# Kernel optimization log

Measured on AMD Instinct MI355X. Metric: run time of the kernel, lower is better.

The kernel has to match this reference:

```python
import jax, jax.numpy as jnp
import numpy as np

N = 50000      # nodes
E = 800000     # edges (before self-loops)
D = 128        # hid_d
H = 8          # heads
C = D // H     # per-head channels
L = 3          # layers
SLOPE = 0.2    # GATv2 leaky_relu negative slope
EPS = 1e-5     # LayerNorm eps


def setup_inputs() -> dict:
    key = jax.random.key(0)
    ks = jax.random.split(key, 8)
    x = jax.random.normal(ks[0], (N, D), dtype=jnp.float32)
    ei = jax.random.randint(ks[1], (2, E), 0, N, dtype=jnp.int32)
    s = 1.0 / np.sqrt(D)
    Wl = jax.random.normal(ks[2], (L, D, D), dtype=jnp.float32) * s   # source transform per layer
    Wr = jax.random.normal(ks[3], (L, D, D), dtype=jnp.float32) * s   # target transform per layer
    att = jax.random.normal(ks[4], (L, H, C), dtype=jnp.float32) * (1.0 / np.sqrt(C))
    bias = jnp.zeros((L, D), dtype=jnp.float32)
    gamma = jnp.ones((L, D), dtype=jnp.float32)
    beta = jnp.zeros((L, D), dtype=jnp.float32)
    return {"x": x, "Wl": Wl, "Wr": Wr, "att": att, "bias": bias,
            "gamma": gamma, "beta": beta, "ei": ei}


def _layernorm(y, g, b):
    mu = jnp.mean(y, axis=-1, keepdims=True)
    var = jnp.mean(jnp.square(y - mu), axis=-1, keepdims=True)
    return (y - mu) * jax.lax.rsqrt(var + EPS) * g + b


def reference(x, Wl, Wr, att, bias, gamma, beta, ei):
    # append self-loops (PyG GATv2Conv default add_self_loops=True)
    loops = jnp.arange(N, dtype=ei.dtype)
    src = jnp.concatenate([ei[0], loops])  # [E+N]
    dst = jnp.concatenate([ei[1], loops])  # [E+N]
    h = x
    for l in range(L):
        xl = (h @ Wl[l]).reshape(N, H, C)   # source-side features
        xr = (h @ Wr[l]).reshape(N, H, C)   # target-side features
        feat = xl[src] + xr[dst]            # [E+N, H, C] per-edge gather
        logits = jnp.einsum('ehc,hc->eh', jax.nn.leaky_relu(feat, SLOPE), att[l])
        # segment softmax over incoming edges of each dst node
        m = jax.ops.segment_max(logits, dst, num_segments=N)
        ex = jnp.exp(logits - m[dst])
        denom = jax.ops.segment_sum(ex, dst, num_segments=N)
        alpha = ex / denom[dst]             # [E+N, H]
        msg = alpha[:, :, None] * xl[src]   # [E+N, H, C]
        out = jax.ops.segment_sum(msg, dst, num_segments=N).reshape(N, H * C) + bias[l]
        # wrapper: h = h + dropout(elu(norm(gat(h)))) ; dropout = identity (eval)
        h = h + jax.nn.elu(_layernorm(out, gamma[l], beta[l]))
    return h
```

## Files before the change

### kernel.cpp

```cpp
#include <hip/hip_runtime.h>
#include <hip/hip_fp16.h>
#include <math.h>

#define N_NODES 50000
#define N_EDGES 800000
#define D 128
#define L 3
#define SLOPE 0.2f
#define LN_EPS 1e-5f
#define ETOT (N_EDGES + N_NODES)
#define SCAN_BLOCKS ((N_NODES + 1023) / 1024)

typedef _Float16 half8 __attribute__((ext_vector_type(8)));
typedef _Float16 h2v  __attribute__((ext_vector_type(2)));
typedef float f32x4 __attribute__((ext_vector_type(4)));


__global__ void rank_hist_kernel(const int* __restrict__ ei, int* __restrict__ counts,
                                 int* __restrict__ rank) {
    int idx = blockIdx.x * blockDim.x + threadIdx.x;
    if (idx >= ETOT) return;
    int d = (idx < N_EDGES) ? ei[N_EDGES + idx] : (idx - N_EDGES);
    rank[idx] = atomicAdd(&counts[d], 1);
}

__global__ __launch_bounds__(1024) void scan1_kernel(const int* __restrict__ counts,
                                                     int* __restrict__ offsets,
                                                     int* __restrict__ bsum) {
    __shared__ int wsum[16];
    int tid = threadIdx.x;
    int lane = tid & 63, w = tid >> 6;
    int i = blockIdx.x * 1024 + tid;
    int v = (i < N_NODES) ? counts[i] : 0;
    int sc = v;
    #pragma unroll
    for (int off = 1; off < 64; off <<= 1) {
        int u = __shfl_up(sc, off);
        if (lane >= off) sc += u;
    }
    if (lane == 63) wsum[w] = sc;
    __syncthreads();
    if (w == 0) {
        int t2 = (lane < 16) ? wsum[lane] : 0;
        #pragma unroll
        for (int off = 1; off < 16; off <<= 1) {
            int u = __shfl_up(t2, off);
            if (lane >= off) t2 += u;
        }
        if (lane < 16) wsum[lane] = t2;
    }
    __syncthreads();
    int wpref = (w == 0) ? 0 : wsum[w - 1];
    if (i < N_NODES) offsets[i] = wpref + sc - v;
    if (tid == 0) bsum[blockIdx.x] = wsum[15];
}

__global__ __launch_bounds__(64) void scan2_kernel(const int* __restrict__ bsum,
                                                   int* __restrict__ bpre) {
    int lane = threadIdx.x;
    int v = (lane < SCAN_BLOCKS) ? bsum[lane] : 0;
    int sc = v;
    #pragma unroll
    for (int off = 1; off < 64; off <<= 1) {
        int u = __shfl_up(sc, off);
        if (lane >= off) sc += u;
    }
    if (lane < SCAN_BLOCKS) bpre[lane] = sc - v;
}

__global__ __launch_bounds__(1024) void scan3_kernel(int* __restrict__ offsets,
                                                     const int* __restrict__ bpre) {
    int i = blockIdx.x * 1024 + threadIdx.x;
    if (i < N_NODES) offsets[i] += bpre[blockIdx.x];
    if (i == 0) offsets[N_NODES] = ETOT;
}

__global__ void scatter_kernel(const int* __restrict__ ei, const int* __restrict__ offsets,
                               const int* __restrict__ rank,
                               unsigned short* __restrict__ sorted16) {
    int idx = blockIdx.x * blockDim.x + threadIdx.x;
    if (idx >= ETOT) return;
    int s, d;
    if (idx < N_EDGES) { s = ei[idx]; d = ei[N_EDGES + idx]; }
    else               { s = d = idx - N_EDGES; }
    sorted16[offsets[d] + rank[idx]] = (unsigned short)s;
}


__global__ __launch_bounds__(256) void wfrag_kernel(const float* __restrict__ Wl,
                                                    const float* __restrict__ Wr,
                                                    _Float16* __restrict__ Wfrag) {
    int u = blockIdx.x * 256 + threadIdx.x;
    if (u >= 3 * 4096) return;
    int lane = u & 63, nt = (u >> 6) & 7, kt = (u >> 9) & 3, y = (u >> 11) & 1, l = u >> 12;
    int r = lane & 15, q = lane >> 4;
    const float* W = (y ? Wr : Wl) + (size_t)l * D * D;
    half8 v;
    #pragma unroll
    for (int j = 0; j < 8; ++j)
        v[j] = (_Float16)W[(kt * 32 + q * 8 + j) * D + nt * 16 + r];
    *(half8*)&Wfrag[(size_t)u * 8] = v;
}


__global__ __launch_bounds__(256) void gemm_mfma_kernel(
        const float* __restrict__ h, const _Float16* __restrict__ WfragL,
        _Float16* __restrict__ xlh, _Float16* __restrict__ xrh) {
    __shared__ half8 Afrag[1024];
    int t = threadIdx.x;
    int row0 = blockIdx.x * 64;
    {
        int kt = t >> 6, q = (t >> 4) & 3, r = t & 15;
        int kc = kt * 4 + q;
        #pragma unroll
        for (int i = 0; i < 4; ++i) {
            int row = row0 + i * 16 + r;
            float4 f0 = make_float4(0.f, 0.f, 0.f, 0.f), f1 = f0;
            if (row < N_NODES) {
                const float* p = &h[(size_t)row * D + kc * 8];
                f0 = *(const float4*)p;
                f1 = *(const float4*)(p + 4);
            }
            half8 v;
            v[0] = (_Float16)f0.x; v[1] = (_Float16)f0.y;
            v[2] = (_Float16)f0.z; v[3] = (_Float16)f0.w;
            v[4] = (_Float16)f1.x; v[5] = (_Float16)f1.y;
            v[6] = (_Float16)f1.z; v[7] = (_Float16)f1.w;
            Afrag[i * 256 + t] = v;
        }
    }
    __syncthreads();
    int w = t >> 6, lane = t & 63;
    f32x4 acc[16];
    #pragma unroll
    for (int i = 0; i < 16; ++i) acc[i] = (f32x4){0.f, 0.f, 0.f, 0.f};
    #pragma unroll
    for (int kt = 0; kt < 4; ++kt) {
        half8 a = Afrag[(w * 4 + kt) * 64 + lane];
        #pragma unroll
        for (int y = 0; y < 2; ++y) {
            #pragma unroll
            for (int nt = 0; nt < 8; ++nt) {
                half8 b = *(const half8*)&WfragL[(size_t)(((y * 4 + kt) * 8 + nt) * 64 + lane) * 8];
                acc[y * 8 + nt] = __builtin_amdgcn_mfma_f32_16x16x32_f16(a, b, acc[y * 8 + nt], 0, 0, 0);
            }
        }
    }
    int rq = lane >> 4, rc = lane & 15;
    int rbase = row0 + w * 16 + rq * 4;
    #pragma unroll
    for (int y = 0; y < 2; ++y) {
        _Float16* out = y ? xrh : xlh;
        #pragma unroll
        for (int nt = 0; nt < 8; ++nt) {
            #pragma unroll
            for (int reg = 0; reg < 4; ++reg) {
                int row = rbase + reg;
                if (row < N_NODES)
                    out[(size_t)row * D + nt * 16 + rc] = (_Float16)acc[y * 8 + nt][reg];
            }
        }
    }
}


__device__ __forceinline__ float head_reduce8(float p) {
    int t;
    t = __builtin_amdgcn_update_dpp(0, __float_as_int(p), 0xB1, 0xF, 0xF, true);
    p += __int_as_float(t);
    t = __builtin_amdgcn_update_dpp(0, __float_as_int(p), 0x4E, 0xF, 0xF, true);
    p += __int_as_float(t);
    t = __builtin_amdgcn_update_dpp(0, __float_as_int(p), 0x141, 0xF, 0xF, true);
    p += __int_as_float(t);
    return p;
}

__device__ __forceinline__ float logit2(h2v v, h2v xrv2, h2v att2, h2v slope2) {
    h2v f  = v + xrv2;
    h2v lf = __builtin_elementwise_max(f, f * slope2);
    return __builtin_amdgcn_fdot2(lf, att2, 0.f, false);
}

__device__ __forceinline__ float2 h2f(h2v v) {
    return make_float2((float)v[0], (float)v[1]);
}

__global__ __launch_bounds__(256) void gat_node_kernel(
        const _Float16* __restrict__ xlh, const _Float16* __restrict__ xrh,
        const int* __restrict__ offsets, const unsigned short* __restrict__ sorted16,
        const float* __restrict__ att_l, const float* __restrict__ bias_l,
        const float* __restrict__ gamma_l, const float* __restrict__ beta_l,
        const float* __restrict__ hin, float* __restrict__ hout) {
    int node = (blockIdx.x * blockDim.x + threadIdx.x) >> 6;
    if (node >= N_NODES) return;
    int lane = threadIdx.x & 63;
    unsigned laneoff = lane * 4u;
    h2v xrv2 = ((const h2v*)xrh)[(size_t)node * 64 + lane];
    float2 attf = *(const float2*)&att_l[2 * lane];
    h2v att2;
    att2[0] = (_Float16)(attf.x * 1.44269504f);
    att2[1] = (_Float16)(attf.y * 1.44269504f);
    h2v slope2;
    slope2[0] = (_Float16)SLOPE;
    slope2[1] = (_Float16)SLOPE;
    int beg = offsets[node], end = offsets[node + 1];
    float s = 0.f, accx = 0.f, accy = 0.f;
    const char* xlb = (const char*)xlh;
    for (int c0 = beg; c0 < end; c0 += 64) {
        int cnt = end - c0; if (cnt > 64) cnt = 64;
        unsigned idx = sorted16[c0 + (lane < cnt ? lane : cnt - 1)];
        unsigned off = idx << 8;
        int j = 0;
        for (; j + 8 <= cnt; j += 8) {
            unsigned o0 = __builtin_amdgcn_readlane(off, j)     + laneoff;
            unsigned o1 = __builtin_amdgcn_readlane(off, j + 1) + laneoff;
            unsigned o2 = __builtin_amdgcn_readlane(off, j + 2) + laneoff;
            unsigned o3 = __builtin_amdgcn_readlane(off, j + 3) + laneoff;
            unsigned o4 = __builtin_amdgcn_readlane(off, j + 4) + laneoff;
            unsigned o5 = __builtin_amdgcn_readlane(off, j + 5) + laneoff;
            unsigned o6 = __builtin_amdgcn_readlane(off, j + 6) + laneoff;
            unsigned o7 = __builtin_amdgcn_readlane(off, j + 7) + laneoff;
            h2v v0 = *(const h2v*)(xlb + o0);
            h2v v1 = *(const h2v*)(xlb + o1);
            h2v v2 = *(const h2v*)(xlb + o2);
            h2v v3 = *(const h2v*)(xlb + o3);
            h2v v4 = *(const h2v*)(xlb + o4);
            h2v v5 = *(const h2v*)(xlb + o5);
            h2v v6 = *(const h2v*)(xlb + o6);
            h2v v7 = *(const h2v*)(xlb + o7);
            float p0 = logit2(v0, xrv2, att2, slope2);
            float p1 = logit2(v1, xrv2, att2, slope2);
            float p2 = logit2(v2, xrv2, att2, slope2);
            float p3 = logit2(v3, xrv2, att2, slope2);
            float p4 = logit2(v4, xrv2, att2, slope2);
            float p5 = logit2(v5, xrv2, att2, slope2);
            float p6 = logit2(v6, xrv2, att2, slope2);
            float p7 = logit2(v7, xrv2, att2, slope2);
            p0 = head_reduce8(p0); p1 = head_reduce8(p1);
            p2 = head_reduce8(p2); p3 = head_reduce8(p3);
            p4 = head_reduce8(p4); p5 = head_reduce8(p5);
            p6 = head_reduce8(p6); p7 = head_reduce8(p7);
            float e0 = __builtin_amdgcn_exp2f(p0), e1 = __builtin_amdgcn_exp2f(p1);
            float e2 = __builtin_amdgcn_exp2f(p2), e3 = __builtin_amdgcn_exp2f(p3);
            float e4 = __builtin_amdgcn_exp2f(p4), e5 = __builtin_amdgcn_exp2f(p5);
            float e6 = __builtin_amdgcn_exp2f(p6), e7 = __builtin_amdgcn_exp2f(p7);
            s += ((e0 + e1) + (e2 + e3)) + ((e4 + e5) + (e6 + e7));
            float2 f0 = h2f(v0), f1 = h2f(v1);
            float2 f2 = h2f(v2), f3 = h2f(v3);
            float2 f4 = h2f(v4), f5 = h2f(v5);
            float2 f6 = h2f(v6), f7 = h2f(v7);
            accx = fmaf(e0, f0.x, accx); accy = fmaf(e0, f0.y, accy);
            accx = fmaf(e1, f1.x, accx); accy = fmaf(e1, f1.y, accy);
            accx = fmaf(e2, f2.x, accx); accy = fmaf(e2, f2.y, accy);
            accx = fmaf(e3, f3.x, accx); accy = fmaf(e3, f3.y, accy);
            accx = fmaf(e4, f4.x, accx); accy = fmaf(e4, f4.y, accy);
            accx = fmaf(e5, f5.x, accx); accy = fmaf(e5, f5.y, accy);
            accx = fmaf(e6, f6.x, accx); accy = fmaf(e6, f6.y, accy);
            accx = fmaf(e7, f7.x, accx); accy = fmaf(e7, f7.y, accy);
        }
        for (; j < cnt; ++j) {
            unsigned o0 = __builtin_amdgcn_readlane(off, j) + laneoff;
            h2v v0 = *(const h2v*)(xlb + o0);
            float p0 = logit2(v0, xrv2, att2, slope2);
            p0 = head_reduce8(p0);
            float e0 = __builtin_amdgcn_exp2f(p0);
            s += e0;
            float2 f0 = h2f(v0);
            accx = fmaf(e0, f0.x, accx);
            accy = fmaf(e0, f0.y, accy);
        }
    }
    float inv = 1.f / s;
    float2 bia = *(const float2*)&bias_l[2 * lane];
    float o0 = accx * inv + bia.x;
    float o1 = accy * inv + bia.y;
    float sum = o0 + o1, sq = o0 * o0 + o1 * o1;
    #pragma unroll
    for (int msk = 1; msk < 64; msk <<= 1) {
        sum += __shfl_xor(sum, msk);
        sq  += __shfl_xor(sq, msk);
    }
    float mu   = sum * (1.f / 128.f);
    float var  = sq * (1.f / 128.f) - mu * mu;
    float rstd = rsqrtf(var + LN_EPS);
    float2 gam = *(const float2*)&gamma_l[2 * lane];
    float2 bet = *(const float2*)&beta_l[2 * lane];
    float y0 = (o0 - mu) * rstd * gam.x + bet.x;
    float y1 = (o1 - mu) * rstd * gam.y + bet.y;
    y0 = y0 > 0.f ? y0 : __expf(y0) - 1.f;
    y1 = y1 > 0.f ? y1 : __expf(y1) - 1.f;
    size_t di = (size_t)node * D + 2 * lane;
    float2 hv = *(const float2*)&hin[di];
    hv.x += y0; hv.y += y1;
    *(float2*)&hout[di] = hv;
}


extern "C" void kernel_launch(void* const* d_in, const int* in_sizes, int n_in,
                              void* d_out, int out_size, void* d_ws, size_t ws_size,
                              hipStream_t stream) {
    const float* x     = (const float*)d_in[0];
    const float* Wl    = (const float*)d_in[1];
    const float* Wr    = (const float*)d_in[2];
    const float* att   = (const float*)d_in[3];
    const float* bias  = (const float*)d_in[4];
    const float* gamma = (const float*)d_in[5];
    const float* beta  = (const float*)d_in[6];
    const int*   ei    = (const int*)d_in[7];
    float* h = (float*)d_out;

    char* ws = (char*)d_ws;
    _Float16* xlh = (_Float16*)ws;   ws += (size_t)N_NODES * D * sizeof(_Float16);
    _Float16* xrh = (_Float16*)ws;   ws += (size_t)N_NODES * D * sizeof(_Float16);
    _Float16* Wfrag = (_Float16*)ws; ws += (size_t)3 * 4096 * 8 * sizeof(_Float16);
    int* offsets = (int*)ws;         ws += (size_t)(N_NODES + 4) * sizeof(int);
    int* counts  = (int*)ws;         ws += (size_t)N_NODES * sizeof(int);
    int* bsum    = (int*)ws;         ws += 64 * sizeof(int);
    int* bpre    = (int*)ws;         ws += 64 * sizeof(int);
    int* rank    = (int*)ws;         ws += (size_t)ETOT * sizeof(int);
    unsigned short* sorted16 = (unsigned short*)ws;

    wfrag_kernel<<<48, 256, 0, stream>>>(Wl, Wr, Wfrag);
    (void)hipMemsetAsync(counts, 0, (size_t)N_NODES * sizeof(int), stream);
    rank_hist_kernel<<<(ETOT + 255) / 256, 256, 0, stream>>>(ei, counts, rank);
    scan1_kernel<<<SCAN_BLOCKS, 1024, 0, stream>>>(counts, offsets, bsum);
    scan2_kernel<<<1, 64, 0, stream>>>(bsum, bpre);
    scan3_kernel<<<SCAN_BLOCKS, 1024, 0, stream>>>(offsets, bpre);
    scatter_kernel<<<(ETOT + 255) / 256, 256, 0, stream>>>(ei, offsets, rank, sorted16);

    for (int l = 0; l < L; ++l) {
        const float* hin = (l == 0) ? x : h;
        gemm_mfma_kernel<<<(N_NODES + 63) / 64, 256, 0, stream>>>(
            hin, Wfrag + (size_t)l * 4096 * 8, xlh, xrh);
        gat_node_kernel<<<(N_NODES * 64 + 255) / 256, 256, 0, stream>>>(
            xlh, xrh, offsets, sorted16,
            att + (size_t)l * D, bias + (size_t)l * D,
            gamma + (size_t)l * D, beta + (size_t)l * D, hin, h);
    }
}
```

Measured before the change: 340.9 us.

## Process two nodes per wavefront with 4 channels per lane in GAT aggregation

Restructures the GAT aggregation kernel so each 64-lane wavefront handles two destination nodes, with 32 lanes per node and each lane loading 8-byte half4 feature chunks. The head reduction shrinks to a 4-lane DPP reduce, the LayerNorm reduce to 32 lanes, and output is written as float4. This is meant to widen per-lane memory accesses and halve the number of waves. In exchange, both half-waves loop to the larger of the two degrees, with masked wasted work when degrees differ.

```diff
diff --git a/kernel.cpp b/kernel.cpp
--- a/kernel.cpp
+++ b/kernel.cpp
@@ -12,6 +12,7 @@
 #define SCAN_BLOCKS ((N_NODES + 1023) / 1024)
 
 typedef _Float16 half8 __attribute__((ext_vector_type(8)));
+typedef _Float16 h4v  __attribute__((ext_vector_type(4)));
 typedef _Float16 h2v  __attribute__((ext_vector_type(2)));
 typedef float f32x4 __attribute__((ext_vector_type(4)));
 
@@ -164,25 +165,25 @@
 }
 
 
-__device__ __forceinline__ float head_reduce8(float p) {
+__device__ __forceinline__ float quad_reduce4(float p) {
     int t;
     t = __builtin_amdgcn_update_dpp(0, __float_as_int(p), 0xB1, 0xF, 0xF, true);
     p += __int_as_float(t);
     t = __builtin_amdgcn_update_dpp(0, __float_as_int(p), 0x4E, 0xF, 0xF, true);
     p += __int_as_float(t);
-    t = __builtin_amdgcn_update_dpp(0, __float_as_int(p), 0x141, 0xF, 0xF, true);
-    p += __int_as_float(t);
     return p;
 }
 
-__device__ __forceinline__ float logit2(h2v v, h2v xrv2, h2v att2, h2v slope2) {
-    h2v f  = v + xrv2;
-    h2v lf = __builtin_elementwise_max(f, f * slope2);
-    return __builtin_amdgcn_fdot2(lf, att2, 0.f, false);
-}
-
-__device__ __forceinline__ float2 h2f(h2v v) {
-    return make_float2((float)v[0], (float)v[1]);
+__device__ __forceinline__ float logit4(h4v v, h2v xrA, h2v xrB, h2v attA, h2v attB,
+                                        h2v slope2) {
+    h2v v0; v0[0] = v[0]; v0[1] = v[1];
+    h2v v1; v1[0] = v[2]; v1[1] = v[3];
+    h2v f0 = v0 + xrA;
+    h2v f1 = v1 + xrB;
+    h2v lf0 = __builtin_elementwise_max(f0, f0 * slope2);
+    h2v lf1 = __builtin_elementwise_max(f1, f1 * slope2);
+    float p = __builtin_amdgcn_fdot2(lf0, attA, 0.f, false);
+    return __builtin_amdgcn_fdot2(lf1, attB, p, false);
 }
 
 __global__ __launch_bounds__(256) void gat_node_kernel(
@@ -191,108 +192,117 @@
         const float* __restrict__ att_l, const float* __restrict__ bias_l,
         const float* __restrict__ gamma_l, const float* __restrict__ beta_l,
         const float* __restrict__ hin, float* __restrict__ hout) {
-    int node = (blockIdx.x * blockDim.x + threadIdx.x) >> 6;
-    if (node >= N_NODES) return;
+    int wid = (blockIdx.x * blockDim.x + threadIdx.x) >> 6;
+    if (wid * 2 >= N_NODES) return;
     int lane = threadIdx.x & 63;
-    unsigned laneoff = lane * 4u;
-    h2v xrv2 = ((const h2v*)xrh)[(size_t)node * 64 + lane];
-    float2 attf = *(const float2*)&att_l[2 * lane];
-    h2v att2;
-    att2[0] = (_Float16)(attf.x * 1.44269504f);
-    att2[1] = (_Float16)(attf.y * 1.44269504f);
-    h2v slope2;
+    int sub = lane >> 5, hl = lane & 31;
+    int node = wid * 2 + sub;
+    unsigned laneoff = hl * 8u;
+
+    h4v xr4 = *(const h4v*)&xrh[(size_t)node * D + hl * 4];
+    h2v xrA; xrA[0] = xr4[0]; xrA[1] = xr4[1];
+    h2v xrB; xrB[0] = xr4[2]; xrB[1] = xr4[3];
+    float4 attf = *(const float4*)&att_l[hl * 4];
+    h2v attA, attB, slope2;
+    attA[0] = (_Float16)(attf.x * 1.44269504f);
+    attA[1] = (_Float16)(attf.y * 1.44269504f);
+    attB[0] = (_Float16)(attf.z * 1.44269504f);
+    attB[1] = (_Float16)(attf.w * 1.44269504f);
     slope2[0] = (_Float16)SLOPE;
     slope2[1] = (_Float16)SLOPE;
+
     int beg = offsets[node], end = offsets[node + 1];
-    float s = 0.f, accx = 0.f, accy = 0.f;
+    int deg = end - beg;
+    int degA = __builtin_amdgcn_readlane(deg, 0);
+    int degB = __builtin_amdgcn_readlane(deg, 32);
+    int degMax = degA > degB ? degA : degB;
+
+    float s = 0.f;
+    float acc0 = 0.f, acc1 = 0.f, acc2 = 0.f, acc3 = 0.f;
     const char* xlb = (const char*)xlh;
-    for (int c0 = beg; c0 < end; c0 += 64) {
-        int cnt = end - c0; if (cnt > 64) cnt = 64;
-        unsigned idx = sorted16[c0 + (lane < cnt ? lane : cnt - 1)];
-        unsigned off = idx << 8;
+
+    for (int c0 = 0; c0 < degMax; c0 += 32) {
+        int rem = deg - c0;
+        int cnt = rem > 32 ? 32 : rem;
+        int cl  = cnt > 0 ? (hl < cnt ? hl : cnt - 1) : 0;
+        int pos = cnt > 0 ? beg + c0 + cl : 0;
+        unsigned off = ((unsigned)sorted16[pos]) << 8;
+        int jmax = degMax - c0; if (jmax > 32) jmax = 32;
         int j = 0;
-        for (; j + 8 <= cnt; j += 8) {
-            unsigned o0 = __builtin_amdgcn_readlane(off, j)     + laneoff;
-            unsigned o1 = __builtin_amdgcn_readlane(off, j + 1) + laneoff;
-            unsigned o2 = __builtin_amdgcn_readlane(off, j + 2) + laneoff;
-            unsigned o3 = __builtin_amdgcn_readlane(off, j + 3) + laneoff;
-            unsigned o4 = __builtin_amdgcn_readlane(off, j + 4) + laneoff;
-            unsigned o5 = __builtin_amdgcn_readlane(off, j + 5) + laneoff;
-            unsigned o6 = __builtin_amdgcn_readlane(off, j + 6) + laneoff;
-            unsigned o7 = __builtin_amdgcn_readlane(off, j + 7) + laneoff;
-            h2v v0 = *(const h2v*)(xlb + o0);
-            h2v v1 = *(const h2v*)(xlb + o1);
-            h2v v2 = *(const h2v*)(xlb + o2);
-            h2v v3 = *(const h2v*)(xlb + o3);
-            h2v v4 = *(const h2v*)(xlb + o4);
-            h2v v5 = *(const h2v*)(xlb + o5);
-            h2v v6 = *(const h2v*)(xlb + o6);
-            h2v v7 = *(const h2v*)(xlb + o7);
-            float p0 = logit2(v0, xrv2, att2, slope2);
-            float p1 = logit2(v1, xrv2, att2, slope2);
-            float p2 = logit2(v2, xrv2, att2, slope2);
-            float p3 = logit2(v3, xrv2, att2, slope2);
-            float p4 = logit2(v4, xrv2, att2, slope2);
-            float p5 = logit2(v5, xrv2, att2, slope2);
-            float p6 = logit2(v6, xrv2, att2, slope2);
-            float p7 = logit2(v7, xrv2, att2, slope2);
-            p0 = head_reduce8(p0); p1 = head_reduce8(p1);
-            p2 = head_reduce8(p2); p3 = head_reduce8(p3);
-            p4 = head_reduce8(p4); p5 = head_reduce8(p5);
-            p6 = head_reduce8(p6); p7 = head_reduce8(p7);
-            float e0 = __builtin_amdgcn_exp2f(p0), e1 = __builtin_amdgcn_exp2f(p1);
-            float e2 = __builtin_amdgcn_exp2f(p2), e3 = __builtin_amdgcn_exp2f(p3);
-            float e4 = __builtin_amdgcn_exp2f(p4), e5 = __builtin_amdgcn_exp2f(p5);
-            float e6 = __builtin_amdgcn_exp2f(p6), e7 = __builtin_amdgcn_exp2f(p7);
-            s += ((e0 + e1) + (e2 + e3)) + ((e4 + e5) + (e6 + e7));
-            float2 f0 = h2f(v0), f1 = h2f(v1);
-            float2 f2 = h2f(v2), f3 = h2f(v3);
-            float2 f4 = h2f(v4), f5 = h2f(v5);
-            float2 f6 = h2f(v6), f7 = h2f(v7);
-            accx = fmaf(e0, f0.x, accx); accy = fmaf(e0, f0.y, accy);
-            accx = fmaf(e1, f1.x, accx); accy = fmaf(e1, f1.y, accy);
-            accx = fmaf(e2, f2.x, accx); accy = fmaf(e2, f2.y, accy);
-            accx = fmaf(e3, f3.x, accx); accy = fmaf(e3, f3.y, accy);
-            accx = fmaf(e4, f4.x, accx); accy = fmaf(e4, f4.y, accy);
-            accx = fmaf(e5, f5.x, accx); accy = fmaf(e5, f5.y, accy);
-            accx = fmaf(e6, f6.x, accx); accy = fmaf(e6, f6.y, accy);
-            accx = fmaf(e7, f7.x, accx); accy = fmaf(e7, f7.y, accy);
-        }
-        for (; j < cnt; ++j) {
-            unsigned o0 = __builtin_amdgcn_readlane(off, j) + laneoff;
-            h2v v0 = *(const h2v*)(xlb + o0);
-            float p0 = logit2(v0, xrv2, att2, slope2);
-            p0 = head_reduce8(p0);
-            float e0 = __builtin_amdgcn_exp2f(p0);
-            s += e0;
-            float2 f0 = h2f(v0);
-            accx = fmaf(e0, f0.x, accx);
-            accy = fmaf(e0, f0.y, accy);
-        }
-    }
+        for (; j + 8 <= jmax; j += 8) {
+            h4v vs[8];
+            #pragma unroll
+            for (int k = 0; k < 8; ++k) {
+                unsigned oA = __builtin_amdgcn_readlane(off, j + k);
+                unsigned oB = __builtin_amdgcn_readlane(off, j + k + 32);
+                unsigned o  = (sub ? oB : oA) + laneoff;
+                vs[k] = *(const h4v*)(xlb + o);
+            }
+            float ems[8];
+            #pragma unroll
+            for (int k = 0; k < 8; ++k) {
+                float p = logit4(vs[k], xrA, xrB, attA, attB, slope2);
+                p = quad_reduce4(p);
+                float e = __builtin_amdgcn_exp2f(p);
+                ems[k] = (j + k < cnt) ? e : 0.f;
+            }
+            s += ((ems[0] + ems[1]) + (ems[2] + ems[3])) +
+                 ((ems[4] + ems[5]) + (ems[6] + ems[7]));
+            #pragma unroll
+            for (int k = 0; k < 8; ++k) {
+                acc0 = fmaf(ems[k], (float)vs[k][0], acc0);
+                acc1 = fmaf(ems[k], (float)vs[k][1], acc1);
+                acc2 = fmaf(ems[k], (float)vs[k][2], acc2);
+                acc3 = fmaf(ems[k], (float)vs[k][3], acc3);
+            }
+        }
+        for (; j < jmax; ++j) {
+            unsigned oA = __builtin_amdgcn_readlane(off, j);
+            unsigned oB = __builtin_amdgcn_readlane(off, j + 32);
+            unsigned o  = (sub ? oB : oA) + laneoff;
+            h4v v = *(const h4v*)(xlb + o);
+            float p = logit4(v, xrA, xrB, attA, attB, slope2);
+            p = quad_reduce4(p);
+            float e = __builtin_amdgcn_exp2f(p);
+            float em = (j < cnt) ? e : 0.f;
+            s += em;
+            acc0 = fmaf(em, (float)v[0], acc0);
+            acc1 = fmaf(em, (float)v[1], acc1);
+            acc2 = fmaf(em, (float)v[2], acc2);
+            acc3 = fmaf(em, (float)v[3], acc3);
+        }
+    }
+
     float inv = 1.f / s;
-    float2 bia = *(const float2*)&bias_l[2 * lane];
-    float o0 = accx * inv + bia.x;
-    float o1 = accy * inv + bia.y;
-    float sum = o0 + o1, sq = o0 * o0 + o1 * o1;
-    #pragma unroll
-    for (int msk = 1; msk < 64; msk <<= 1) {
+    float4 bia = *(const float4*)&bias_l[hl * 4];
+    float o0 = acc0 * inv + bia.x;
+    float o1 = acc1 * inv + bia.y;
+    float o2 = acc2 * inv + bia.z;
+    float o3 = acc3 * inv + bia.w;
+    float sum = (o0 + o1) + (o2 + o3);
+    float sq  = (o0 * o0 + o1 * o1) + (o2 * o2 + o3 * o3);
+    #pragma unroll
+    for (int msk = 1; msk < 32; msk <<= 1) {
         sum += __shfl_xor(sum, msk);
         sq  += __shfl_xor(sq, msk);
     }
     float mu   = sum * (1.f / 128.f);
     float var  = sq * (1.f / 128.f) - mu * mu;
     float rstd = rsqrtf(var + LN_EPS);
-    float2 gam = *(const float2*)&gamma_l[2 * lane];
-    float2 bet = *(const float2*)&beta_l[2 * lane];
+    float4 gam = *(const float4*)&gamma_l[hl * 4];
+    float4 bet = *(const float4*)&beta_l[hl * 4];
     float y0 = (o0 - mu) * rstd * gam.x + bet.x;
     float y1 = (o1 - mu) * rstd * gam.y + bet.y;
+    float y2 = (o2 - mu) * rstd * gam.z + bet.z;
+    float y3 = (o3 - mu) * rstd * gam.w + bet.w;
     y0 = y0 > 0.f ? y0 : __expf(y0) - 1.f;
     y1 = y1 > 0.f ? y1 : __expf(y1) - 1.f;
-    size_t di = (size_t)node * D + 2 * lane;
-    float2 hv = *(const float2*)&hin[di];
-    hv.x += y0; hv.y += y1;
-    *(float2*)&hout[di] = hv;
+    y2 = y2 > 0.f ? y2 : __expf(y2) - 1.f;
+    y3 = y3 > 0.f ? y3 : __expf(y3) - 1.f;
+    size_t di = (size_t)node * D + hl * 4;
+    float4 hv = *(const float4*)&hin[di];
+    hv.x += y0; hv.y += y1; hv.z += y2; hv.w += y3;
+    *(float4*)&hout[di] = hv;
 }
 
 
@@ -328,11 +338,13 @@
     scan3_kernel<<<SCAN_BLOCKS, 1024, 0, stream>>>(offsets, bpre);
     scatter_kernel<<<(ETOT + 255) / 256, 256, 0, stream>>>(ei, offsets, rank, sorted16);
 
+    int gat_waves  = (N_NODES + 1) / 2;
+    int gat_blocks = (gat_waves * 64 + 255) / 256;
     for (int l = 0; l < L; ++l) {
         const float* hin = (l == 0) ? x : h;
         gemm_mfma_kernel<<<(N_NODES + 63) / 64, 256, 0, stream>>>(
             hin, Wfrag + (size_t)l * 4096 * 8, xlh, xrh);
-        gat_node_kernel<<<(N_NODES * 64 + 255) / 256, 256, 0, stream>>>(
+        gat_node_kernel<<<gat_blocks, 256, 0, stream>>>(
             xlh, xrh, offsets, sorted16,
             att + (size_t)l * D, bias + (size_t)l * D,
             gamma + (size_t)l * D, beta + (size_t)l * D, hin, h);
```

Result: faster. 325.2 us (-4.6%).
